# Performance work log

Measured on AMD Instinct MI355X. Metric: run time of the kernel, lower is better.

The kernel has to match this reference:

```python
import jax, jax.numpy as jnp
import numpy as np

GROUPS = 32
EPS = 1e-5


def group_norm(x, scale, bias):
    # x: [b, v, t, s, f]; normalize per (b,v,t) sample over (channels_in_group, s)
    b, v, t, s, f = x.shape
    xg = x.reshape(b, v, t, s, GROUPS, f // GROUPS)
    mean = xg.mean(axis=(3, 5), keepdims=True)
    var = xg.var(axis=(3, 5), keepdims=True)
    xn = ((xg - mean) * jax.lax.rsqrt(var + EPS)).reshape(b, v, t, s, f)
    return xn * scale + bias


def nh_conv(x, adjc, W, b):
    # x: [b,v,t,s,f_in]; adjc: [s, k]; W: [k, f_in, f_out]; b: [f_out]
    x_nh = x[:, :, :, adjc, :]                      # [b,v,t,s,k,f_in]
    return jnp.einsum('bvtskf,kfo->bvtso', x_nh, W) + b


def setup_inputs() -> dict:
    key = jax.random.key(0)
    ks = jax.random.split(key, 12)
    B, V, T, S, F_IN, F_OUT, K = 1, 2, 2, 12288, 128, 256, 9
    x = jax.random.normal(ks[0], (B, V, T, S, F_IN), dtype=jnp.float32)
    adjc = jax.random.randint(ks[1], (S, K), 0, S, dtype=jnp.int32)
    gn1_scale = jnp.ones((F_IN,), jnp.float32)
    gn1_bias = jnp.zeros((F_IN,), jnp.float32)
    gn2_scale = jnp.ones((F_OUT,), jnp.float32)
    gn2_bias = jnp.zeros((F_OUT,), jnp.float32)
    W_skip = jax.random.normal(ks[2], (F_IN, F_OUT), jnp.float32) / np.sqrt(F_IN)
    b_skip = jnp.zeros((F_OUT,), jnp.float32)
    W1 = jax.random.normal(ks[3], (K, F_IN, F_OUT), jnp.float32) / np.sqrt(K * F_IN)
    b1 = jnp.zeros((F_OUT,), jnp.float32)
    W2 = jax.random.normal(ks[4], (K, F_OUT, F_OUT), jnp.float32) / np.sqrt(K * F_OUT)
    b2 = jnp.zeros((F_OUT,), jnp.float32)
    return dict(x=x, adjc=adjc, gn1_scale=gn1_scale, gn1_bias=gn1_bias,
                gn2_scale=gn2_scale, gn2_bias=gn2_bias, W_skip=W_skip, b_skip=b_skip,
                W1=W1, b1=b1, W2=W2, b2=b2)


def reference(x, gn1_scale, gn1_bias, gn2_scale, gn2_bias, W_skip, b_skip,
              W1, b1, W2, b2, adjc):
    # skip_layer: ProjLayer with zoom_diff=0 -> plain Linear in->out
    x_res = jnp.einsum('bvtsf,fo->bvtso', x, W_skip) + b_skip
    # norm1 + SiLU (updownconv is Identity when zooms match and in==in feats)
    h = jax.nn.silu(group_norm(x, gn1_scale, gn1_bias))
    # conv1: neighbor-gather linear [k, f_in] -> f_out
    h = nh_conv(h, adjc, W1, b1)
    # emb_layer = Identity; norm2 + SiLU
    h = jax.nn.silu(group_norm(h, gn2_scale, gn2_bias))
    # conv2 + residual
    h = nh_conv(h, adjc, W2, b2)
    return h + x_res
```

## Files before the change

kernel.cpp:

```cpp
#include <hip/hip_runtime.h>
#include <hip/hip_bf16.h>

typedef __bf16 bf16_t;
typedef __bf16 bf16x8 __attribute__((ext_vector_type(8)));
typedef float f32x4 __attribute__((ext_vector_type(4)));
typedef int i32x4 __attribute__((ext_vector_type(4)));

#define S_TOT 12288
#define F_IN 128
#define F_OUT 256
#define EPS 1e-5f

static __device__ __forceinline__ float silu_f(float v) {
  return v / (1.0f + __expf(-v));
}

static __device__ __forceinline__ void gll16(const bf16_t* g, bf16_t* l) {
  __builtin_amdgcn_global_load_lds(
      (const __attribute__((address_space(1))) void*)(const void*)g,
      (__attribute__((address_space(3))) void*)(void*)l, 16, 0, 0);
}

__global__ void prep_kernel(const float* __restrict__ W1,
                            const float* __restrict__ W2,
                            const float* __restrict__ Wsk,
                            bf16_t* __restrict__ W1p,
                            bf16_t* __restrict__ W2p,
                            bf16_t* __restrict__ Wsp,
                            const float* __restrict__ x,
                            float* __restrict__ sum1, float* __restrict__ ss1) {
  __shared__ float gs[32], gq[32];
  if (blockIdx.x < 448) {
    int w = blockIdx.x * 4 + (threadIdx.x >> 6);
    int l = threadIdx.x & 63;
    int lo = l & 15, hi = l >> 4;
    const float* src;
    bf16_t* dst;
    int fbase, obase;
    if (w < 576) {
      int kcg = w >> 4, cb = w & 15;
      int tap = kcg % 9, chunk = kcg / 9;
      src = W1 + tap * 32768;
      dst = W1p + (size_t)w * 512;
      fbase = 32 * chunk + 8 * hi; obase = 16 * cb + lo;
    } else if (w < 1728) {
      int idx = w - 576;
      int kcg = idx >> 4, cb = idx & 15;
      int tap = kcg % 9, chunk = kcg / 9;
      src = W2 + tap * 65536;
      dst = W2p + (size_t)idx * 512;
      fbase = 32 * chunk + 8 * hi; obase = 16 * cb + lo;
    } else {
      int idx = w - 1728;
      int kc = idx >> 4, cb = idx & 15;
      src = Wsk;
      dst = Wsp + (size_t)idx * 512;
      fbase = 32 * kc + 8 * hi; obase = 16 * cb + lo;
    }
    bf16x8 v;
#pragma unroll
    for (int j = 0; j < 8; ++j)
      v[j] = (bf16_t)src[(fbase + j) * 256 + obase];
    *(bf16x8*)(dst + l * 8) = v;
  } else {
    int blk = blockIdx.x - 448;
    int vt = blk & 3;
    int s0 = (blk >> 2) * 256;
    int t = threadIdx.x;
    int col = t & 31, ro = t >> 5;
    float s_ = 0.f, q_ = 0.f;
    const f32x4* xp = (const f32x4*)(x + ((size_t)vt * S_TOT + s0) * F_IN);
#pragma unroll 4
    for (int it = 0; it < 32; ++it) {
      f32x4 v = xp[(size_t)(it * 8 + ro) * 32 + col];
      s_ += v[0] + v[1] + v[2] + v[3];
      q_ += v[0]*v[0] + v[1]*v[1] + v[2]*v[2] + v[3]*v[3];
    }
    if (t < 32) { gs[t] = 0.f; gq[t] = 0.f; }
    __syncthreads();
    atomicAdd(&gs[col], s_);
    atomicAdd(&gq[col], q_);
    __syncthreads();
    if (t < 32) {
      atomicAdd(&sum1[vt * 32 + t], gs[t]);
      atomicAdd(&ss1[vt * 32 + t], gq[t]);
    }
  }
}

__global__ void apply_gn1(const float* __restrict__ x,
                          const float* __restrict__ sum1, const float* __restrict__ ss1,
                          const float* __restrict__ gs, const float* __restrict__ gb,
                          bf16_t* __restrict__ h1) {
  size_t base = ((size_t)blockIdx.x * 256 + threadIdx.x) * 8;
  int vt = (int)(base / ((size_t)S_TOT * F_IN));
  int c0 = (int)(base & (F_IN - 1));
  const f32x4* xp = (const f32x4*)(x + base);
  f32x4 v0 = xp[0], v1 = xp[1];
  float N = (float)(S_TOT * 4);
  bf16x8 o;
#pragma unroll
  for (int gi = 0; gi < 2; ++gi) {
    int g = (c0 >> 2) + gi;
    float mean = sum1[vt * 32 + g] / N;
    float var = ss1[vt * 32 + g] / N - mean * mean;
    float r = rsqrtf(var + EPS);
    f32x4 v = gi ? v1 : v0;
#pragma unroll
    for (int j = 0; j < 4; ++j) {
      int c = g * 4 + j;
      float a = r * gs[c];
      float b = gb[c] - mean * a;
      o[gi * 4 + j] = (bf16_t)silu_f(v[j] * a + b);
    }
  }
  *(bf16x8*)(h1 + base) = o;
}

__global__ void apply_gn2(bf16_t* __restrict__ h,
                          const float* __restrict__ sum_c, const float* __restrict__ ss_c,
                          const float* __restrict__ gs, const float* __restrict__ gb) {
  size_t base = ((size_t)blockIdx.x * 256 + threadIdx.x) * 8;
  int vt = (int)(base / ((size_t)S_TOT * F_OUT));
  int c0 = (int)(base & (F_OUT - 1));
  int g = c0 >> 3;
  bf16x8 v = *(const bf16x8*)(h + base);
  float sg = 0.f, qg = 0.f;
#pragma unroll
  for (int j = 0; j < 8; ++j) {
    sg += sum_c[vt * 256 + g * 8 + j];
    qg += ss_c[vt * 256 + g * 8 + j];
  }
  float N = (float)(S_TOT * 8);
  float mean = sg / N;
  float var = qg / N - mean * mean;
  float r = rsqrtf(var + EPS);
  bf16x8 o;
#pragma unroll
  for (int j = 0; j < 8; ++j) {
    int c = g * 8 + j;
    float a = r * gs[c];
    float b = gb[c] - mean * a;
    o[j] = (bf16_t)silu_f((float)v[j] * a + b);
  }
  *(bf16x8*)(h + base) = o;
}

template<int RE, int NSUB, bool XSK>
__global__ __launch_bounds__(256, 3) void conv_kernel(
    const bf16_t* __restrict__ hsrc, const bf16_t* __restrict__ Wp,
    const bf16_t* __restrict__ Wsp, const float* __restrict__ x,
    const int* __restrict__ adjc, const float* __restrict__ bias,
    const float* __restrict__ biask, bf16_t* __restrict__ outb,
    float* __restrict__ outf, float* __restrict__ sum_c, float* __restrict__ ss_c) {
  const int tid = threadIdx.x;
  const int wv = tid >> 6, l = tid & 63;
  const int lo = l & 15, hi = l >> 4;
  const int nw = wv;

  int swz = ((blockIdx.x & 7) * 96) + (blockIdx.x >> 3);
  int vt = swz / 192;
  int rem = swz - vt * 192;
  int s0 = rem * 64;

  __shared__ int adjs[576];
  __shared__ bf16_t ab[3][2048];

  for (int i = tid; i < 576; i += 256) adjs[i] = adjc[s0 * 9 + i];
  __syncthreads();

  const bf16_t* hb = hsrc + (size_t)vt * ((size_t)S_TOT * RE);
  constexpr int NMAIN = XSK ? (NSUB - 4) : NSUB;
  const int off = (blockIdx.x >> 8) * (NMAIN / 3);
  auto phys = [&](int k) { int p = k + off; if (p >= NMAIN) p -= NMAIN; return p; };

  auto stageA = [&](int buf, int p) {
    int tap = p % 9, chunk = p / 9;
    int row = wv * 16 + (l >> 2);
    int segs = (l & 3) ^ ((row >> 1) & 3);
    const bf16_t* g = hb + (size_t)adjs[row * 9 + tap] * RE + chunk * 32 + segs * 8;
    gll16(g, &ab[buf][wv * 512]);
  };

  auto asmB = [&](i32x4* dst, const bf16_t* wsrc, int kcg) {
    const bf16_t* p = wsrc + (size_t)kcg * 8192 + nw * 2048 + l * 8;
    asm volatile(
        "global_load_dwordx4 %0, %4, off\n\t"
        "global_load_dwordx4 %1, %4, off offset:1024\n\t"
        "global_load_dwordx4 %2, %4, off offset:2048\n\t"
        "global_load_dwordx4 %3, %4, off offset:3072"
        : "=&v"(dst[0]), "=&v"(dst[1]), "=&v"(dst[2]), "=&v"(dst[3])
        : "v"(p));
  };

  auto stageX = [&](int buf, int sx) {
    int row = tid >> 2, q = tid & 3;
    const float* xr = x + ((size_t)vt * S_TOT + s0 + row) * F_IN + sx * 32 + q * 8;
    f32x4 xv0 = *(const f32x4*)(xr);
    f32x4 xv1 = *(const f32x4*)(xr + 4);
    bf16x8 w;
#pragma unroll
    for (int jj = 0; jj < 4; ++jj) {
      w[jj] = (bf16_t)xv0[jj];
      w[4 + jj] = (bf16_t)xv1[jj];
    }
    *(bf16x8*)(&ab[buf][row * 32 + ((q ^ ((row >> 1) & 3)) << 3)]) = w;
  };

  f32x4 acc[4][4] = {};
  auto compute = [&](int buf, const i32x4* bv) {
    bf16x8 afr[4];
#pragma unroll
    for (int mi = 0; mi < 4; ++mi) {
      int rr = mi * 16 + lo;
      afr[mi] = *(const bf16x8*)(&ab[buf][rr * 32 + ((hi ^ ((rr >> 1) & 3)) << 3)]);
    }
    __builtin_amdgcn_s_setprio(1);
#pragma unroll
    for (int mi = 0; mi < 4; ++mi)
#pragma unroll
      for (int ni = 0; ni < 4; ++ni)
        acc[mi][ni] = __builtin_amdgcn_mfma_f32_16x16x32_bf16(
            afr[mi], __builtin_bit_cast(bf16x8, bv[ni]), acc[mi][ni], 0, 0, 0);
    __builtin_amdgcn_s_setprio(0);
  };

  i32x4 b0[4], b1[4];
  stageA(0, phys(0));
  asmB(b0, Wp, phys(0));
  stageA(1, phys(1));
  int bcur3 = 0, bstg3 = 2;

  for (int s = 0; s < NMAIN - 2; s += 2) {
    asmB(b1, Wp, phys(s + 1));
    asm volatile("s_waitcnt vmcnt(5)" ::: "memory");
    __builtin_amdgcn_s_barrier();
    __builtin_amdgcn_sched_barrier(0);
    stageA(bstg3, phys(s + 2));
    compute(bcur3, b0);
    bcur3 = (bcur3 == 2) ? 0 : bcur3 + 1;
    bstg3 = (bstg3 == 2) ? 0 : bstg3 + 1;
    asmB(b0, Wp, phys(s + 2));
    asm volatile("s_waitcnt vmcnt(5)" ::: "memory");
    __builtin_amdgcn_s_barrier();
    __builtin_amdgcn_sched_barrier(0);
    stageA(bstg3, phys(s + 3));
    compute(bcur3, b1);
    bcur3 = (bcur3 == 2) ? 0 : bcur3 + 1;
    bstg3 = (bstg3 == 2) ? 0 : bstg3 + 1;
  }
  asmB(b1, Wp, phys(NMAIN - 1));
  asm volatile("s_waitcnt vmcnt(5)" ::: "memory");
  __builtin_amdgcn_s_barrier();
  __builtin_amdgcn_sched_barrier(0);
  compute(bcur3, b0);
  bcur3 = (bcur3 == 2) ? 0 : bcur3 + 1;
  asm volatile("s_waitcnt vmcnt(0)" ::: "memory");
  __builtin_amdgcn_s_barrier();
  __builtin_amdgcn_sched_barrier(0);
  compute(bcur3, b1);

  if (XSK) {
#pragma unroll
    for (int sx = 0; sx < 4; ++sx) {
      int tb = sx & 1;
      __syncthreads();
      stageX(tb, sx);
      if (sx & 1) asmB(b1, Wsp, sx); else asmB(b0, Wsp, sx);
      asm volatile("s_waitcnt vmcnt(0)" ::: "memory");
      __syncthreads();
      __builtin_amdgcn_sched_barrier(0);
      compute(tb, (sx & 1) ? (const i32x4*)b1 : (const i32x4*)b0);
    }
  }

  if (!XSK) {
    bf16_t* ob = outb + ((size_t)vt * S_TOT + s0) * 256;
#pragma unroll
    for (int ni = 0; ni < 4; ++ni) {
      int o = nw * 64 + ni * 16 + lo;
      float bv = bias[o];
      float s_ = 0.f, q_ = 0.f;
#pragma unroll
      for (int mi = 0; mi < 4; ++mi)
#pragma unroll
        for (int r2 = 0; r2 < 4; ++r2) {
          int srow = mi * 16 + hi * 4 + r2;
          float v = acc[mi][ni][r2] + bv;
          ob[(size_t)srow * 256 + o] = (bf16_t)v;
          s_ += v; q_ += v * v;
        }
      s_ += __shfl_xor(s_, 16); s_ += __shfl_xor(s_, 32);
      q_ += __shfl_xor(q_, 16); q_ += __shfl_xor(q_, 32);
      if (hi == 0) {
        atomicAdd(&sum_c[vt * 256 + o], s_);
        atomicAdd(&ss_c[vt * 256 + o], q_);
      }
    }
  } else {
    float* of = outf + ((size_t)vt * S_TOT + s0) * 256;
#pragma unroll
    for (int ni = 0; ni < 4; ++ni) {
      int o = nw * 64 + ni * 16 + lo;
      float bv = bias[o] + biask[o];
#pragma unroll
      for (int mi = 0; mi < 4; ++mi)
#pragma unroll
        for (int r2 = 0; r2 < 4; ++r2) {
          int srow = mi * 16 + hi * 4 + r2;
          of[(size_t)srow * 256 + o] = acc[mi][ni][r2] + bv;
        }
    }
  }
}

extern "C" void kernel_launch(void* const* d_in, const int* in_sizes, int n_in,
                              void* d_out, int out_size, void* d_ws, size_t ws_size,
                              hipStream_t stream) {
  const float* x      = (const float*)d_in[0];
  const int*   adjc   = (const int*)d_in[1];
  const float* gn1_s  = (const float*)d_in[2];
  const float* gn1_b  = (const float*)d_in[3];
  const float* gn2_s  = (const float*)d_in[4];
  const float* gn2_b  = (const float*)d_in[5];
  const float* W_skip = (const float*)d_in[6];
  const float* b_skip = (const float*)d_in[7];
  const float* W1     = (const float*)d_in[8];
  const float* b1     = (const float*)d_in[9];
  const float* W2     = (const float*)d_in[10];
  const float* b2     = (const float*)d_in[11];
  float* out = (float*)d_out;

  float* sum1  = (float*)d_ws;
  float* ss1   = sum1 + 128;
  float* sum_c = ss1 + 128;
  float* ss_c  = sum_c + 1024;
  float* pad   = ss_c + 1024;
  bf16_t* W1p  = (bf16_t*)(pad + 3072);
  bf16_t* W2p  = W1p + 294912;
  bf16_t* Wsp  = W2p + 589824;
  bf16_t* h1   = Wsp + 32768;
  bf16_t* out1 = h1 + 6291456;

  hipMemsetAsync(sum1, 0, (128 + 128 + 1024 + 1024) * sizeof(float), stream);
  prep_kernel<<<640, 256, 0, stream>>>(W1, W2, W_skip, W1p, W2p, Wsp, x, sum1, ss1);
  apply_gn1<<<3072, 256, 0, stream>>>(x, sum1, ss1, gn1_s, gn1_b, h1);
  conv_kernel<128, 36, false><<<768, 256, 0, stream>>>(
      h1, W1p, nullptr, nullptr, adjc, b1, nullptr, out1, nullptr, sum_c, ss_c);
  apply_gn2<<<6144, 256, 0, stream>>>(out1, sum_c, ss_c, gn2_s, gn2_b);
  conv_kernel<256, 76, true><<<768, 256, 0, stream>>>(
      out1, W2p, Wsp, x, adjc, b2, b_skip, nullptr, out, nullptr, nullptr);
}
```

Measured before the change: 143.7 us.

## Double K-step depth per pipeline stage to 64 channels in conv kernel

Each pipeline stage of the conv kernel now covers 64 input channels (two 32-channel subchunks) per tap instead of 32. That halves the number of barriers and waitcnt rounds and issues larger gathers per stage. It also drops the rotating start offset across blocks that spread weight-tile access. In exchange it doubles LDS staging buffers and B-fragment registers (8 i32x4 per set), which may pressure occupancy at launch_bounds(256,3).

Result: faster. 137.5 us (-4.3%).

```diff
diff --git a/kernel.cpp b/kernel.cpp
--- a/kernel.cpp
+++ b/kernel.cpp
@@ -146,7 +146,7 @@
   *(bf16x8*)(h + base) = o;
 }
 
-template<int RE, int NSUB, bool XSK>
+template<int RE, int NM64, bool XSK>
 __global__ __launch_bounds__(256, 3) void conv_kernel(
     const bf16_t* __restrict__ hsrc, const bf16_t* __restrict__ Wp,
     const bf16_t* __restrict__ Wsp, const float* __restrict__ x,
@@ -164,93 +164,125 @@
   int s0 = rem * 64;
 
   __shared__ int adjs[576];
-  __shared__ bf16_t ab[3][2048];
+  __shared__ bf16_t ab[3][2][2048];
 
   for (int i = tid; i < 576; i += 256) adjs[i] = adjc[s0 * 9 + i];
   __syncthreads();
 
   const bf16_t* hb = hsrc + (size_t)vt * ((size_t)S_TOT * RE);
-  constexpr int NMAIN = XSK ? (NSUB - 4) : NSUB;
-  const int off = (blockIdx.x >> 8) * (NMAIN / 3);
-  auto phys = [&](int k) { int p = k + off; if (p >= NMAIN) p -= NMAIN; return p; };
-
-  auto stageA = [&](int buf, int p) {
-    int tap = p % 9, chunk = p / 9;
+
+  auto stageA = [&](int buf, int i) {
+    int tap = i % 9, cpair = i / 9;
     int row = wv * 16 + (l >> 2);
     int segs = (l & 3) ^ ((row >> 1) & 3);
-    const bf16_t* g = hb + (size_t)adjs[row * 9 + tap] * RE + chunk * 32 + segs * 8;
-    gll16(g, &ab[buf][wv * 512]);
-  };
-
-  auto asmB = [&](i32x4* dst, const bf16_t* wsrc, int kcg) {
-    const bf16_t* p = wsrc + (size_t)kcg * 8192 + nw * 2048 + l * 8;
+    const bf16_t* g = hb + (size_t)adjs[row * 9 + tap] * RE + cpair * 64 + segs * 8;
+    gll16(g, &ab[buf][0][wv * 512]);
+    gll16(g + 32, &ab[buf][1][wv * 512]);
+  };
+
+  auto asmB = [&](i32x4* dst, int i) {
+    int tap = i % 9, cpair = i / 9;
+    const bf16_t* pa = Wp + (size_t)(18 * cpair + tap) * 8192 + nw * 2048 + l * 8;
+    const bf16_t* pb = pa + 9 * 8192;
     asm volatile(
         "global_load_dwordx4 %0, %4, off\n\t"
         "global_load_dwordx4 %1, %4, off offset:1024\n\t"
         "global_load_dwordx4 %2, %4, off offset:2048\n\t"
         "global_load_dwordx4 %3, %4, off offset:3072"
         : "=&v"(dst[0]), "=&v"(dst[1]), "=&v"(dst[2]), "=&v"(dst[3])
-        : "v"(p));
+        : "v"(pa));
+    asm volatile(
+        "global_load_dwordx4 %0, %4, off\n\t"
+        "global_load_dwordx4 %1, %4, off offset:1024\n\t"
+        "global_load_dwordx4 %2, %4, off offset:2048\n\t"
+        "global_load_dwordx4 %3, %4, off offset:3072"
+        : "=&v"(dst[4]), "=&v"(dst[5]), "=&v"(dst[6]), "=&v"(dst[7])
+        : "v"(pb));
+  };
+
+  auto asmBx = [&](i32x4* dst, int sx) {
+    const bf16_t* pa = Wsp + (size_t)(2 * sx) * 8192 + nw * 2048 + l * 8;
+    const bf16_t* pb = pa + 8192;
+    asm volatile(
+        "global_load_dwordx4 %0, %4, off\n\t"
+        "global_load_dwordx4 %1, %4, off offset:1024\n\t"
+        "global_load_dwordx4 %2, %4, off offset:2048\n\t"
+        "global_load_dwordx4 %3, %4, off offset:3072"
+        : "=&v"(dst[0]), "=&v"(dst[1]), "=&v"(dst[2]), "=&v"(dst[3])
+        : "v"(pa));
+    asm volatile(
+        "global_load_dwordx4 %0, %4, off\n\t"
+        "global_load_dwordx4 %1, %4, off offset:1024\n\t"
+        "global_load_dwordx4 %2, %4, off offset:2048\n\t"
+        "global_load_dwordx4 %3, %4, off offset:3072"
+        : "=&v"(dst[4]), "=&v"(dst[5]), "=&v"(dst[6]), "=&v"(dst[7])
+        : "v"(pb));
   };
 
   auto stageX = [&](int buf, int sx) {
     int row = tid >> 2, q = tid & 3;
-    const float* xr = x + ((size_t)vt * S_TOT + s0 + row) * F_IN + sx * 32 + q * 8;
-    f32x4 xv0 = *(const f32x4*)(xr);
-    f32x4 xv1 = *(const f32x4*)(xr + 4);
-    bf16x8 w;
-#pragma unroll
-    for (int jj = 0; jj < 4; ++jj) {
-      w[jj] = (bf16_t)xv0[jj];
-      w[4 + jj] = (bf16_t)xv1[jj];
-    }
-    *(bf16x8*)(&ab[buf][row * 32 + ((q ^ ((row >> 1) & 3)) << 3)]) = w;
+    const float* xr = x + ((size_t)vt * S_TOT + s0 + row) * F_IN + sx * 64 + q * 8;
+#pragma unroll
+    for (int sc = 0; sc < 2; ++sc) {
+      f32x4 xv0 = *(const f32x4*)(xr + sc * 32);
+      f32x4 xv1 = *(const f32x4*)(xr + sc * 32 + 4);
+      bf16x8 w;
+#pragma unroll
+      for (int jj = 0; jj < 4; ++jj) {
+        w[jj] = (bf16_t)xv0[jj];
+        w[4 + jj] = (bf16_t)xv1[jj];
+      }
+      *(bf16x8*)(&ab[buf][sc][row * 32 + ((q ^ ((row >> 1) & 3)) << 3)]) = w;
+    }
   };
 
   f32x4 acc[4][4] = {};
   auto compute = [&](int buf, const i32x4* bv) {
-    bf16x8 afr[4];
-#pragma unroll
-    for (int mi = 0; mi < 4; ++mi) {
-      int rr = mi * 16 + lo;
-      afr[mi] = *(const bf16x8*)(&ab[buf][rr * 32 + ((hi ^ ((rr >> 1) & 3)) << 3)]);
-    }
     __builtin_amdgcn_s_setprio(1);
 #pragma unroll
-    for (int mi = 0; mi < 4; ++mi)
-#pragma unroll
-      for (int ni = 0; ni < 4; ++ni)
-        acc[mi][ni] = __builtin_amdgcn_mfma_f32_16x16x32_bf16(
-            afr[mi], __builtin_bit_cast(bf16x8, bv[ni]), acc[mi][ni], 0, 0, 0);
+    for (int sc = 0; sc < 2; ++sc) {
+      bf16x8 afr[4];
+#pragma unroll
+      for (int mi = 0; mi < 4; ++mi) {
+        int rr = mi * 16 + lo;
+        afr[mi] = *(const bf16x8*)(&ab[buf][sc][rr * 32 + ((hi ^ ((rr >> 1) & 3)) << 3)]);
+      }
+#pragma unroll
+      for (int mi = 0; mi < 4; ++mi)
+#pragma unroll
+        for (int ni = 0; ni < 4; ++ni)
+          acc[mi][ni] = __builtin_amdgcn_mfma_f32_16x16x32_bf16(
+              afr[mi], __builtin_bit_cast(bf16x8, bv[sc * 4 + ni]), acc[mi][ni], 0, 0, 0);
+    }
     __builtin_amdgcn_s_setprio(0);
   };
 
-  i32x4 b0[4], b1[4];
-  stageA(0, phys(0));
-  asmB(b0, Wp, phys(0));
-  stageA(1, phys(1));
+  i32x4 b0[8], b1[8];
+  stageA(0, 0);
+  asmB(b0, 0);
+  stageA(1, 1);
   int bcur3 = 0, bstg3 = 2;
 
-  for (int s = 0; s < NMAIN - 2; s += 2) {
-    asmB(b1, Wp, phys(s + 1));
-    asm volatile("s_waitcnt vmcnt(5)" ::: "memory");
+  for (int s = 0; s < NM64 - 2; s += 2) {
+    asmB(b1, s + 1);
+    asm volatile("s_waitcnt vmcnt(10)" ::: "memory");
     __builtin_amdgcn_s_barrier();
     __builtin_amdgcn_sched_barrier(0);
-    stageA(bstg3, phys(s + 2));
+    stageA(bstg3, s + 2);
     compute(bcur3, b0);
     bcur3 = (bcur3 == 2) ? 0 : bcur3 + 1;
     bstg3 = (bstg3 == 2) ? 0 : bstg3 + 1;
-    asmB(b0, Wp, phys(s + 2));
-    asm volatile("s_waitcnt vmcnt(5)" ::: "memory");
+    asmB(b0, s + 2);
+    asm volatile("s_waitcnt vmcnt(10)" ::: "memory");
     __builtin_amdgcn_s_barrier();
     __builtin_amdgcn_sched_barrier(0);
-    stageA(bstg3, phys(s + 3));
+    stageA(bstg3, s + 3);
     compute(bcur3, b1);
     bcur3 = (bcur3 == 2) ? 0 : bcur3 + 1;
     bstg3 = (bstg3 == 2) ? 0 : bstg3 + 1;
   }
-  asmB(b1, Wp, phys(NMAIN - 1));
-  asm volatile("s_waitcnt vmcnt(5)" ::: "memory");
+  asmB(b1, NM64 - 1);
+  asm volatile("s_waitcnt vmcnt(10)" ::: "memory");
   __builtin_amdgcn_s_barrier();
   __builtin_amdgcn_sched_barrier(0);
   compute(bcur3, b0);
@@ -262,15 +294,14 @@
 
   if (XSK) {
 #pragma unroll
-    for (int sx = 0; sx < 4; ++sx) {
-      int tb = sx & 1;
+    for (int sx = 0; sx < 2; ++sx) {
       __syncthreads();
-      stageX(tb, sx);
-      if (sx & 1) asmB(b1, Wsp, sx); else asmB(b0, Wsp, sx);
+      stageX(sx, sx);
+      if (sx) asmBx(b1, sx); else asmBx(b0, sx);
       asm volatile("s_waitcnt vmcnt(0)" ::: "memory");
       __syncthreads();
       __builtin_amdgcn_sched_barrier(0);
-      compute(tb, (sx & 1) ? (const i32x4*)b1 : (const i32x4*)b0);
+      compute(sx, sx ? (const i32x4*)b1 : (const i32x4*)b0);
     }
   }
 
@@ -345,9 +376,9 @@
   hipMemsetAsync(sum1, 0, (128 + 128 + 1024 + 1024) * sizeof(float), stream);
   prep_kernel<<<640, 256, 0, stream>>>(W1, W2, W_skip, W1p, W2p, Wsp, x, sum1, ss1);
   apply_gn1<<<3072, 256, 0, stream>>>(x, sum1, ss1, gn1_s, gn1_b, h1);
-  conv_kernel<128, 36, false><<<768, 256, 0, stream>>>(
+  conv_kernel<128, 18, false><<<768, 256, 0, stream>>>(
       h1, W1p, nullptr, nullptr, adjc, b1, nullptr, out1, nullptr, sum_c, ss_c);
   apply_gn2<<<6144, 256, 0, stream>>>(out1, sum_c, ss_c, gn2_s, gn2_b);
-  conv_kernel<256, 76, true><<<768, 256, 0, stream>>>(
+  conv_kernel<256, 36, true><<<768, 256, 0, stream>>>(
       out1, W2p, Wsp, x, adjc, b2, b_skip, nullptr, out, nullptr, nullptr);
 }
```
